# Optimization experiments

Hardware: AMD Instinct MI355X
Metric: run time of the kernel (lower is better)

Reference implementation:

```python
import jax, jax.numpy as jnp
import numpy as np

# AdaptiveLIF neuron constants (tau_mem=20, tau_thresh=60 from __init__)
TAU_MEM = 20.0
TAU_THRESH = 60.0
TH_BASE = 1.0      # resting threshold
TH_INC = 0.1       # threshold increment per spike (adaptation)
SG_SLOPE = 4.0     # surrogate-gradient sigmoid slope


def _spike(u):
    """Heaviside forward, sigmoid surrogate gradient (straight-through)."""
    sig = jax.nn.sigmoid(SG_SLOPE * u)
    hard = (u >= 0).astype(u.dtype)
    return jax.lax.stop_gradient(hard - sig) + sig


def setup_inputs() -> dict:
    key = jax.random.key(0)
    k1, k2, k3 = jax.random.split(key, 3)
    B, N, FIN, FOUT = 2, 8192, 128, 128
    x = jax.random.normal(k1, (B, N, FIN), dtype=jnp.float32)
    # dense adjacency, roughly row-normalized so pre-activations are O(1)
    adj = jax.random.uniform(k2, (B, N, N), dtype=jnp.float32) * (2.0 / N)
    weight = jax.random.normal(k3, (FIN, FOUT), dtype=jnp.float32) * (1.0 / np.sqrt(FIN))
    bias = jnp.zeros((FOUT,), dtype=jnp.float32)
    return {"x": x, "adj": adj, "weight": weight, "bias": bias, "time_steps": 5}


def reference(x, adj, weight, bias, time_steps):
    # support = x @ W ; output = adj @ support + b  -> constant drive I per step
    support = jnp.einsum('bnf,fg->bng', x, weight)          # [B,N,Fout]
    I = jnp.einsum('bnm,bmg->bng', adj, support) + bias     # [B,N,Fout]

    mem_decay = 1.0 - 1.0 / TAU_MEM

    # Fused recurrence: instead of materializing the repeated 4D tensor,
    # scan the adaptive-LIF state and accumulate the spike sum in-carry.
    def step(carry, _):
        v, th, acc = carry
        v = v * mem_decay + I                     # leaky integration
        s = _spike(v - th)                        # threshold crossing
        v = v * (1.0 - s)                         # reset on spike
        th = th + (TH_BASE - th) / TAU_THRESH + TH_INC * s  # adaptive threshold
        return (v, th, acc + s), None

    v0 = jnp.zeros_like(I)
    th0 = jnp.full_like(I, TH_BASE)
    acc0 = jnp.zeros_like(I)
    (_, _, acc), _ = jax.lax.scan(step, (v0, th0, acc0), None, length=time_steps)
    return acc / float(time_steps)                # mean over time -> [B,N,Fout]
```

## Files before the change

### kernel.cpp

```cpp
#include <hip/hip_runtime.h>
#include <math.h>

typedef __attribute__((ext_vector_type(8))) short short8;
typedef __attribute__((ext_vector_type(4))) float f32x4;

static __device__ __forceinline__ unsigned short f2bf(float f) {
  unsigned int u = __float_as_uint(f);
  u = u + 0x7fffu + ((u >> 16) & 1u);
  return (unsigned short)(u >> 16);
}

__global__ __launch_bounds__(256) void support_kernel(
    const float* __restrict__ x, const float* __restrict__ w,
    unsigned short* __restrict__ supT, int N) {
  __shared__ float aT[64][65];
  __shared__ float bs[64][132];

  const int tid = threadIdx.x;
  const long long r0 = (long long)blockIdx.x * 64;
  const float* Ab = x + r0 * 128;
  const int tx = tid & 15;
  const int ty = tid >> 4;

  float acc[4][8] = {};
  const int ar = tid & 63, ak = (tid >> 6) * 16;
  const int bk = tid >> 2, bc = (tid & 3) * 32;

  for (int k0 = 0; k0 < 128; k0 += 64) {
    const float4* asrc = (const float4*)(Ab + (long long)ar * 128 + k0 + ak);
    #pragma unroll
    for (int j = 0; j < 4; ++j) {
      float4 v = asrc[j];
      aT[ak + 4*j + 0][ar] = v.x;
      aT[ak + 4*j + 1][ar] = v.y;
      aT[ak + 4*j + 2][ar] = v.z;
      aT[ak + 4*j + 3][ar] = v.w;
    }
    const float4* bsrc = (const float4*)(w + (long long)(k0 + bk) * 128 + bc);
    #pragma unroll
    for (int j = 0; j < 8; ++j) *(float4*)&bs[bk][bc + 4*j] = bsrc[j];
    __syncthreads();
    #pragma unroll 16
    for (int k = 0; k < 64; ++k) {
      float a[4], b[8];
      *(float4*)a      = *(const float4*)&aT[k][ty*4];
      *(float4*)&b[0]  = *(const float4*)&bs[k][tx*8];
      *(float4*)&b[4]  = *(const float4*)&bs[k][tx*8 + 4];
      #pragma unroll
      for (int i = 0; i < 4; ++i)
        #pragma unroll
        for (int j = 0; j < 8; ++j)
          acc[i][j] = fmaf(a[i], b[j], acc[i][j]);
    }
    __syncthreads();
  }
  const int batch = (int)(r0 / N);
  const int nloc = (int)(r0 % N) + ty * 4;
  #pragma unroll
  for (int j = 0; j < 8; ++j) {
    const int col = tx * 8 + j;
    ushort4 pv;
    pv.x = f2bf(acc[0][j]); pv.y = f2bf(acc[1][j]);
    pv.z = f2bf(acc[2][j]); pv.w = f2bf(acc[3][j]);
    *(ushort4*)&supT[(size_t)batch * 128 * N + (size_t)col * N + nloc] = pv;
  }
}

#define BK2 128
#define ASTR (BK2 + 8)

__global__ __launch_bounds__(256) void spike_gemm_kernel(
    const float* __restrict__ adj, const unsigned short* __restrict__ supT,
    const float* __restrict__ bias, const int* __restrict__ tsp,
    float* __restrict__ out, int N) {
  __shared__ __align__(16) unsigned short As[32][ASTR];

  const int tid = threadIdx.x;
  const int lane = tid & 63;
  const int wave = tid >> 6;
  const int batch = blockIdx.y;
  const int n0 = blockIdx.x * 32;

  const float* Ab = adj + ((size_t)batch * N + n0) * N;
  const unsigned short* Bb = supT + (size_t)batch * 128 * N;

  const int ar = tid >> 4;
  const int akq = tid & 15;

  const int fm = lane & 15;
  const int kg = lane >> 4;

  f32x4 acc[2][2] = {};

  for (int k0 = 0; k0 < N; k0 += BK2) {
    uint4 bfr[2][4];
    #pragma unroll
    for (int ct = 0; ct < 2; ++ct) {
      const unsigned short* bp =
          Bb + (size_t)(wave * 32 + ct * 16 + fm) * N + k0 + kg * 8;
      #pragma unroll
      for (int ks = 0; ks < 4; ++ks)
        bfr[ct][ks] = *(const uint4*)(bp + ks * 32);
    }
    #pragma unroll
    for (int r = 0; r < 2; ++r) {
      const float* ap = Ab + (size_t)(ar + r * 16) * N + k0 + akq * 8;
      float4 v0 = *(const float4*)ap;
      float4 v1 = *(const float4*)(ap + 4);
      ushort4 p0, p1;
      p0.x = f2bf(v0.x); p0.y = f2bf(v0.y); p0.z = f2bf(v0.z); p0.w = f2bf(v0.w);
      p1.x = f2bf(v1.x); p1.y = f2bf(v1.y); p1.z = f2bf(v1.z); p1.w = f2bf(v1.w);
      ushort4* dst = (ushort4*)&As[ar + r * 16][akq * 8];
      dst[0] = p0; dst[1] = p1;
    }
    __syncthreads();
    #pragma unroll
    for (int ks = 0; ks < 4; ++ks) {
      short8 a0 = *(const short8*)&As[fm][ks * 32 + kg * 8];
      short8 a1 = *(const short8*)&As[16 + fm][ks * 32 + kg * 8];
      #pragma unroll
      for (int ct = 0; ct < 2; ++ct) {
        short8 b = *(const short8*)&bfr[ct][ks];
        acc[0][ct] = __builtin_amdgcn_mfma_f32_16x16x32_bf16(a0, b, acc[0][ct], 0, 0, 0);
        acc[1][ct] = __builtin_amdgcn_mfma_f32_16x16x32_bf16(a1, b, acc[1][ct], 0, 0, 0);
      }
    }
    __syncthreads();
  }

  const int T = *tsp;
  #pragma unroll
  for (int rt = 0; rt < 2; ++rt) {
    #pragma unroll
    for (int ct = 0; ct < 2; ++ct) {
      const int col = wave * 32 + ct * 16 + fm;
      const float bv = bias[col];
      #pragma unroll
      for (int i = 0; i < 4; ++i) {
        float I = acc[rt][ct][i] + bv;
        float v = 0.0f, th = 1.0f, sacc = 0.0f;
        for (int t = 0; t < T; ++t) {
          v = v * 0.95f + I;
          float u = v - th;
          float sig = 1.0f / (1.0f + expf(-4.0f * u));
          float hard = (u >= 0.0f) ? 1.0f : 0.0f;
          float s = (hard - sig) + sig;
          sacc += s;
          v = v * (1.0f - s);
          th = th + (1.0f - th) / 60.0f + 0.1f * s;
        }
        const int row = n0 + rt * 16 + kg * 4 + i;
        out[((size_t)batch * N + row) * 128 + col] = sacc / (float)T;
      }
    }
  }
}

extern "C" void kernel_launch(void* const* d_in, const int* in_sizes, int n_in,
                              void* d_out, int out_size, void* d_ws, size_t ws_size,
                              hipStream_t stream) {
  const float* x    = (const float*)d_in[0];
  const float* adj  = (const float*)d_in[1];
  const float* w    = (const float*)d_in[2];
  const float* bias = (const float*)d_in[3];
  const int*   tsp  = (const int*)d_in[4];
  float* out = (float*)d_out;
  unsigned short* supT = (unsigned short*)d_ws;

  const long long sz_x = in_sizes[0];
  const long long sz_adj = in_sizes[1];
  const int N = (int)(sz_adj / sz_x * 128);
  const int B = (int)(sz_x / ((long long)N * 128));
  const int rows = B * N;

  support_kernel<<<rows / 64, 256, 0, stream>>>(x, w, supT, N);
  spike_gemm_kernel<<<dim3(N / 32, B), 256, 0, stream>>>(adj, supT, bias, tsp, out, N);
}
```

Measured before the change: 734.7 us.

## Double-buffer adj tile in LDS with prefetch and halve row tile

Splits the adjacency-times-support GEMM into 16-row tiles and double-buffers the bf16-converted adj tile in shared memory. The next tile's global loads are issued before the MFMAs, and only one barrier remains per iteration. Launch bounds request higher occupancy and the grid doubles. The aim is to hide global load latency, at the cost of reloading the support matrix twice as often per output row.

```diff
diff --git a/kernel.cpp b/kernel.cpp
--- a/kernel.cpp
+++ b/kernel.cpp
@@ -66,92 +66,104 @@
   }
 }
 
-#define BK2 128
-#define ASTR (BK2 + 8)
+#define BK 128
+#define ASTR 136
 
-__global__ __launch_bounds__(256) void spike_gemm_kernel(
+__global__ __launch_bounds__(256, 4) void spike_gemm_kernel(
     const float* __restrict__ adj, const unsigned short* __restrict__ supT,
     const float* __restrict__ bias, const int* __restrict__ tsp,
     float* __restrict__ out, int N) {
-  __shared__ __align__(16) unsigned short As[32][ASTR];
+  __shared__ __align__(16) short As[2][16][ASTR];
 
   const int tid = threadIdx.x;
   const int lane = tid & 63;
   const int wave = tid >> 6;
   const int batch = blockIdx.y;
-  const int n0 = blockIdx.x * 32;
+  const int n0 = blockIdx.x * 16;
 
   const float* Ab = adj + ((size_t)batch * N + n0) * N;
   const unsigned short* Bb = supT + (size_t)batch * 128 * N;
 
   const int ar = tid >> 4;
-  const int akq = tid & 15;
+  const int ac = (tid & 15) * 8;
+  const float* aRow = Ab + (size_t)ar * N + ac;
 
   const int fm = lane & 15;
   const int kg = lane >> 4;
+  const unsigned short* b0 = Bb + (size_t)(wave * 32 + fm) * N + kg * 8;
+  const unsigned short* b1 = b0 + (size_t)16 * N;
 
-  f32x4 acc[2][2] = {};
+  f32x4 acc[2] = {};
 
-  for (int k0 = 0; k0 < N; k0 += BK2) {
+  const int NIT = N / BK;
+
+  {
+    float4 v0 = *(const float4*)(aRow);
+    float4 v1 = *(const float4*)(aRow + 4);
+    short8 pk;
+    pk[0] = (short)f2bf(v0.x); pk[1] = (short)f2bf(v0.y);
+    pk[2] = (short)f2bf(v0.z); pk[3] = (short)f2bf(v0.w);
+    pk[4] = (short)f2bf(v1.x); pk[5] = (short)f2bf(v1.y);
+    pk[6] = (short)f2bf(v1.z); pk[7] = (short)f2bf(v1.w);
+    *(short8*)&As[0][ar][ac] = pk;
+  }
+
+  for (int it = 0; it < NIT; ++it) {
+    __syncthreads();
+    const int cur = it & 1;
+    const int k0 = it * BK;
+
+    float4 p0, p1;
+    if (it + 1 < NIT) {
+      p0 = *(const float4*)(aRow + k0 + BK);
+      p1 = *(const float4*)(aRow + k0 + BK + 4);
+    }
+
     uint4 bfr[2][4];
     #pragma unroll
-    for (int ct = 0; ct < 2; ++ct) {
-      const unsigned short* bp =
-          Bb + (size_t)(wave * 32 + ct * 16 + fm) * N + k0 + kg * 8;
-      #pragma unroll
-      for (int ks = 0; ks < 4; ++ks)
-        bfr[ct][ks] = *(const uint4*)(bp + ks * 32);
+    for (int ks = 0; ks < 4; ++ks) {
+      bfr[0][ks] = *(const uint4*)(b0 + k0 + ks * 32);
+      bfr[1][ks] = *(const uint4*)(b1 + k0 + ks * 32);
     }
-    #pragma unroll
-    for (int r = 0; r < 2; ++r) {
-      const float* ap = Ab + (size_t)(ar + r * 16) * N + k0 + akq * 8;
-      float4 v0 = *(const float4*)ap;
-      float4 v1 = *(const float4*)(ap + 4);
-      ushort4 p0, p1;
-      p0.x = f2bf(v0.x); p0.y = f2bf(v0.y); p0.z = f2bf(v0.z); p0.w = f2bf(v0.w);
-      p1.x = f2bf(v1.x); p1.y = f2bf(v1.y); p1.z = f2bf(v1.z); p1.w = f2bf(v1.w);
-      ushort4* dst = (ushort4*)&As[ar + r * 16][akq * 8];
-      dst[0] = p0; dst[1] = p1;
-    }
-    __syncthreads();
+
     #pragma unroll
     for (int ks = 0; ks < 4; ++ks) {
-      short8 a0 = *(const short8*)&As[fm][ks * 32 + kg * 8];
-      short8 a1 = *(const short8*)&As[16 + fm][ks * 32 + kg * 8];
-      #pragma unroll
-      for (int ct = 0; ct < 2; ++ct) {
-        short8 b = *(const short8*)&bfr[ct][ks];
-        acc[0][ct] = __builtin_amdgcn_mfma_f32_16x16x32_bf16(a0, b, acc[0][ct], 0, 0, 0);
-        acc[1][ct] = __builtin_amdgcn_mfma_f32_16x16x32_bf16(a1, b, acc[1][ct], 0, 0, 0);
-      }
+      short8 a = *(const short8*)&As[cur][fm][ks * 32 + kg * 8];
+      acc[0] = __builtin_amdgcn_mfma_f32_16x16x32_bf16(a, *(const short8*)&bfr[0][ks], acc[0], 0, 0, 0);
+      acc[1] = __builtin_amdgcn_mfma_f32_16x16x32_bf16(a, *(const short8*)&bfr[1][ks], acc[1], 0, 0, 0);
     }
-    __syncthreads();
+
+    if (it + 1 < NIT) {
+      short8 pk;
+      pk[0] = (short)f2bf(p0.x); pk[1] = (short)f2bf(p0.y);
+      pk[2] = (short)f2bf(p0.z); pk[3] = (short)f2bf(p0.w);
+      pk[4] = (short)f2bf(p1.x); pk[5] = (short)f2bf(p1.y);
+      pk[6] = (short)f2bf(p1.z); pk[7] = (short)f2bf(p1.w);
+      *(short8*)&As[cur ^ 1][ar][ac] = pk;
+    }
   }
 
   const int T = *tsp;
   #pragma unroll
-  for (int rt = 0; rt < 2; ++rt) {
+  for (int ct = 0; ct < 2; ++ct) {
+    const int col = wave * 32 + ct * 16 + fm;
+    const float bv = bias[col];
     #pragma unroll
-    for (int ct = 0; ct < 2; ++ct) {
-      const int col = wave * 32 + ct * 16 + fm;
-      const float bv = bias[col];
-      #pragma unroll
-      for (int i = 0; i < 4; ++i) {
-        float I = acc[rt][ct][i] + bv;
-        float v = 0.0f, th = 1.0f, sacc = 0.0f;
-        for (int t = 0; t < T; ++t) {
-          v = v * 0.95f + I;
-          float u = v - th;
-          float sig = 1.0f / (1.0f + expf(-4.0f * u));
-          float hard = (u >= 0.0f) ? 1.0f : 0.0f;
-          float s = (hard - sig) + sig;
-          sacc += s;
-          v = v * (1.0f - s);
-          th = th + (1.0f - th) / 60.0f + 0.1f * s;
-        }
-        const int row = n0 + rt * 16 + kg * 4 + i;
-        out[((size_t)batch * N + row) * 128 + col] = sacc / (float)T;
+    for (int i = 0; i < 4; ++i) {
+      float I = acc[ct][i] + bv;
+      float v = 0.0f, th = 1.0f, sacc = 0.0f;
+      for (int t = 0; t < T; ++t) {
+        v = v * 0.95f + I;
+        float u = v - th;
+        float sig = 1.0f / (1.0f + expf(-4.0f * u));
+        float hard = (u >= 0.0f) ? 1.0f : 0.0f;
+        float s = (hard - sig) + sig;
+        sacc += s;
+        v = v * (1.0f - s);
+        th = th + (1.0f - th) / 60.0f + 0.1f * s;
       }
+      const int row = n0 + kg * 4 + i;
+      out[((size_t)batch * N + row) * 128 + col] = sacc / (float)T;
     }
   }
 }
@@ -174,5 +186,5 @@
   const int rows = B * N;
 
   support_kernel<<<rows / 64, 256, 0, stream>>>(x, w, supT, N);
-  spike_gemm_kernel<<<dim3(N / 32, B), 256, 0, stream>>>(adj, supT, bias, tsp, out, N);
+  spike_gemm_kernel<<<dim3(N / 16, B), 256, 0, stream>>>(adj, supT, bias, tsp, out, N);
 }
```

New measurement: 855.4 us. 1.16x slower.

## Drop LDS staging in spike GEMM, load A/B fragments directly with register prefetch

Applied to the files above, without the earlier changes.

The adjacency GEMM no longer stages bf16-converted A tiles through shared memory with two barriers per K step. Each wave now loads its own A row fragment straight from global memory in MFMA layout, converts it in registers, and double-buffers A and B fragments one K step ahead. The wave tiling changes from 32 rows x 32 cols per wave to 16 rows x 64 cols per wave. This removes the LDS traffic and syncs, but each A row is now read by two waves and every lane makes narrow strided global loads, which could hurt coalescing on this memory-bound adj stream.

```diff
diff --git a/kernel.cpp b/kernel.cpp
--- a/kernel.cpp
+++ b/kernel.cpp
@@ -8,6 +8,15 @@
   unsigned int u = __float_as_uint(f);
   u = u + 0x7fffu + ((u >> 16) & 1u);
   return (unsigned short)(u >> 16);
+}
+
+static __device__ __forceinline__ short8 pack_bf16(float4 v0, float4 v1) {
+  short8 r;
+  r[0] = (short)f2bf(v0.x); r[1] = (short)f2bf(v0.y);
+  r[2] = (short)f2bf(v0.z); r[3] = (short)f2bf(v0.w);
+  r[4] = (short)f2bf(v1.x); r[5] = (short)f2bf(v1.y);
+  r[6] = (short)f2bf(v1.z); r[7] = (short)f2bf(v1.w);
+  return r;
 }
 
 __global__ __launch_bounds__(256) void support_kernel(
@@ -66,92 +75,87 @@
   }
 }
 
-#define BK2 128
-#define ASTR (BK2 + 8)
-
 __global__ __launch_bounds__(256) void spike_gemm_kernel(
     const float* __restrict__ adj, const unsigned short* __restrict__ supT,
     const float* __restrict__ bias, const int* __restrict__ tsp,
     float* __restrict__ out, int N) {
-  __shared__ __align__(16) unsigned short As[32][ASTR];
-
   const int tid = threadIdx.x;
   const int lane = tid & 63;
   const int wave = tid >> 6;
   const int batch = blockIdx.y;
   const int n0 = blockIdx.x * 32;
 
-  const float* Ab = adj + ((size_t)batch * N + n0) * N;
-  const unsigned short* Bb = supT + (size_t)batch * 128 * N;
-
-  const int ar = tid >> 4;
-  const int akq = tid & 15;
-
   const int fm = lane & 15;
   const int kg = lane >> 4;
 
-  f32x4 acc[2][2] = {};
+  const int arow = n0 + (wave >> 1) * 16 + fm;
+  const int cbase = (wave & 1) * 64;
 
-  for (int k0 = 0; k0 < N; k0 += BK2) {
-    uint4 bfr[2][4];
-    #pragma unroll
-    for (int ct = 0; ct < 2; ++ct) {
-      const unsigned short* bp =
-          Bb + (size_t)(wave * 32 + ct * 16 + fm) * N + k0 + kg * 8;
-      #pragma unroll
-      for (int ks = 0; ks < 4; ++ks)
-        bfr[ct][ks] = *(const uint4*)(bp + ks * 32);
-    }
-    #pragma unroll
-    for (int r = 0; r < 2; ++r) {
-      const float* ap = Ab + (size_t)(ar + r * 16) * N + k0 + akq * 8;
-      float4 v0 = *(const float4*)ap;
-      float4 v1 = *(const float4*)(ap + 4);
-      ushort4 p0, p1;
-      p0.x = f2bf(v0.x); p0.y = f2bf(v0.y); p0.z = f2bf(v0.z); p0.w = f2bf(v0.w);
-      p1.x = f2bf(v1.x); p1.y = f2bf(v1.y); p1.z = f2bf(v1.z); p1.w = f2bf(v1.w);
-      ushort4* dst = (ushort4*)&As[ar + r * 16][akq * 8];
-      dst[0] = p0; dst[1] = p1;
-    }
-    __syncthreads();
-    #pragma unroll
-    for (int ks = 0; ks < 4; ++ks) {
-      short8 a0 = *(const short8*)&As[fm][ks * 32 + kg * 8];
-      short8 a1 = *(const short8*)&As[16 + fm][ks * 32 + kg * 8];
-      #pragma unroll
-      for (int ct = 0; ct < 2; ++ct) {
-        short8 b = *(const short8*)&bfr[ct][ks];
-        acc[0][ct] = __builtin_amdgcn_mfma_f32_16x16x32_bf16(a0, b, acc[0][ct], 0, 0, 0);
-        acc[1][ct] = __builtin_amdgcn_mfma_f32_16x16x32_bf16(a1, b, acc[1][ct], 0, 0, 0);
-      }
-    }
-    __syncthreads();
+  const float* ap = adj + ((size_t)batch * N + arow) * N + kg * 8;
+  const unsigned short* Bk = supT + (size_t)batch * 128 * N + kg * 8;
+  const unsigned short* bp0 = Bk + (size_t)(cbase +  0 + fm) * N;
+  const unsigned short* bp1 = Bk + (size_t)(cbase + 16 + fm) * N;
+  const unsigned short* bp2 = Bk + (size_t)(cbase + 32 + fm) * N;
+  const unsigned short* bp3 = Bk + (size_t)(cbase + 48 + fm) * N;
+
+  f32x4 acc[4] = {};
+  const int NK = N / 32;
+
+  float4 a0 = *(const float4*)(ap);
+  float4 a1 = *(const float4*)(ap + 4);
+  uint4 b0 = *(const uint4*)(bp0);
+  uint4 b1 = *(const uint4*)(bp1);
+  uint4 b2 = *(const uint4*)(bp2);
+  uint4 b3 = *(const uint4*)(bp3);
+
+  #pragma unroll 4
+  for (int ks = 0; ks < NK - 1; ++ks) {
+    const int off = (ks + 1) * 32;
+    float4 na0 = *(const float4*)(ap + off);
+    float4 na1 = *(const float4*)(ap + off + 4);
+    uint4 nb0 = *(const uint4*)(bp0 + off);
+    uint4 nb1 = *(const uint4*)(bp1 + off);
+    uint4 nb2 = *(const uint4*)(bp2 + off);
+    uint4 nb3 = *(const uint4*)(bp3 + off);
+
+    short8 a = pack_bf16(a0, a1);
+    acc[0] = __builtin_amdgcn_mfma_f32_16x16x32_bf16(a, *(const short8*)&b0, acc[0], 0, 0, 0);
+    acc[1] = __builtin_amdgcn_mfma_f32_16x16x32_bf16(a, *(const short8*)&b1, acc[1], 0, 0, 0);
+    acc[2] = __builtin_amdgcn_mfma_f32_16x16x32_bf16(a, *(const short8*)&b2, acc[2], 0, 0, 0);
+    acc[3] = __builtin_amdgcn_mfma_f32_16x16x32_bf16(a, *(const short8*)&b3, acc[3], 0, 0, 0);
+
+    a0 = na0; a1 = na1;
+    b0 = nb0; b1 = nb1; b2 = nb2; b3 = nb3;
+  }
+  {
+    short8 a = pack_bf16(a0, a1);
+    acc[0] = __builtin_amdgcn_mfma_f32_16x16x32_bf16(a, *(const short8*)&b0, acc[0], 0, 0, 0);
+    acc[1] = __builtin_amdgcn_mfma_f32_16x16x32_bf16(a, *(const short8*)&b1, acc[1], 0, 0, 0);
+    acc[2] = __builtin_amdgcn_mfma_f32_16x16x32_bf16(a, *(const short8*)&b2, acc[2], 0, 0, 0);
+    acc[3] = __builtin_amdgcn_mfma_f32_16x16x32_bf16(a, *(const short8*)&b3, acc[3], 0, 0, 0);
   }
 
   const int T = *tsp;
   #pragma unroll
-  for (int rt = 0; rt < 2; ++rt) {
+  for (int ct = 0; ct < 4; ++ct) {
+    const int col = cbase + ct * 16 + fm;
+    const float bv = bias[col];
     #pragma unroll
-    for (int ct = 0; ct < 2; ++ct) {
-      const int col = wave * 32 + ct * 16 + fm;
-      const float bv = bias[col];
-      #pragma unroll
-      for (int i = 0; i < 4; ++i) {
-        float I = acc[rt][ct][i] + bv;
-        float v = 0.0f, th = 1.0f, sacc = 0.0f;
-        for (int t = 0; t < T; ++t) {
-          v = v * 0.95f + I;
-          float u = v - th;
-          float sig = 1.0f / (1.0f + expf(-4.0f * u));
-          float hard = (u >= 0.0f) ? 1.0f : 0.0f;
-          float s = (hard - sig) + sig;
-          sacc += s;
-          v = v * (1.0f - s);
-          th = th + (1.0f - th) / 60.0f + 0.1f * s;
-        }
-        const int row = n0 + rt * 16 + kg * 4 + i;
-        out[((size_t)batch * N + row) * 128 + col] = sacc / (float)T;
+    for (int i = 0; i < 4; ++i) {
+      float I = acc[ct][i] + bv;
+      float v = 0.0f, th = 1.0f, sacc = 0.0f;
+      for (int t = 0; t < T; ++t) {
+        v = v * 0.95f + I;
+        float u = v - th;
+        float sig = 1.0f / (1.0f + expf(-4.0f * u));
+        float hard = (u >= 0.0f) ? 1.0f : 0.0f;
+        float s = (hard - sig) + sig;
+        sacc += s;
+        v = v * (1.0f - s);
+        th = th + (1.0f - th) / 60.0f + 0.1f * s;
       }
+      const int row = n0 + (wave >> 1) * 16 + kg * 4 + i;
+      out[((size_t)batch * N + row) * 128 + col] = sacc / (float)T;
     }
   }
 }
```

After: 960.6 us. +30.7%, slower.
